# Optimization experiments

Hardware: AMD Instinct MI355X
Metric: run time of the kernel (lower is better)

The kernel has to match this reference:

```python
import jax, jax.numpy as jnp
import numpy as np

IN_F = 3072       # in_features
OUT_F = 9216      # out_features = 3 * N_HEADS * HEAD_DIM (fused QKV)
GROUP = 64        # quantization group size
RANK = 32         # lora_rank
HEAD_DIM = 128
N_HEADS = OUT_F // (3 * HEAD_DIM)  # 24
EPS = 1e-6
LORA_SCALE = 1.0


def setup_inputs() -> dict:
    key = jax.random.key(0)
    ks = jax.random.split(key, 10)
    B, S = 1, 4096
    x = jax.random.normal(ks[0], (B, S, IN_F), dtype=jnp.float32)
    # packed int4 weights: two signed int4 values per int8 byte
    qweight = jax.random.randint(ks[1], (OUT_F, IN_F // 2), -128, 128, dtype=jnp.int32).astype(jnp.int8)
    wscales = (jax.random.uniform(ks[2], (IN_F // GROUP, OUT_F)) * 0.02 + 0.001).astype(jnp.float32)
    bias = (jax.random.normal(ks[3], (OUT_F,)) * 0.01).astype(jnp.float32)
    lora_down = (jax.random.normal(ks[4], (IN_F, RANK)) * 0.02).astype(jnp.float32)
    lora_up = (jax.random.normal(ks[5], (OUT_F, RANK)) * 0.02).astype(jnp.float32)
    smooth = (jax.random.uniform(ks[6], (IN_F,)) * 0.5 + 0.75).astype(jnp.float32)   # keep away from 0
    norm_q = (jax.random.uniform(ks[7], (HEAD_DIM,)) * 0.5 + 0.75).astype(jnp.float32)
    norm_k = (jax.random.uniform(ks[8], (HEAD_DIM,)) * 0.5 + 0.75).astype(jnp.float32)
    ang = jax.random.uniform(ks[9], (S, HEAD_DIM // 2)) * (2.0 * np.pi)
    rotary_emb = jnp.stack([jnp.cos(ang), jnp.sin(ang)], axis=-1).astype(jnp.float32)  # [S, D/2, 2]
    return dict(x=x, qweight=qweight, wscales=wscales, bias=bias, lora_down=lora_down,
                lora_up=lora_up, smooth=smooth, norm_q=norm_q, norm_k=norm_k, rotary_emb=rotary_emb)


def _dequant_weight(qweight, wscales):
    # unpack two signed int4 lanes from each int8 (low nibble first), then per-group scale
    low = jnp.right_shift(jnp.left_shift(qweight, 4), 4)   # arithmetic shifts on int8 -> sign extend
    high = jnp.right_shift(qweight, 4)
    w4 = jnp.stack([low, high], axis=-1).reshape(OUT_F, IN_F)          # int4 codes in [-8, 7]
    wg = w4.astype(jnp.float32).reshape(OUT_F, IN_F // GROUP, GROUP)
    return (wg * wscales.T[:, :, None]).reshape(OUT_F, IN_F)          # [N, K]


def _quantize_act(x, smooth, lora_down):
    # fused: smooth -> symmetric per-token per-group int4 quantize -> lora_down projection
    B, S, K = x.shape
    M = B * S
    xs = (x / smooth).reshape(M, K)
    xg = xs.reshape(M, K // GROUP, GROUP)
    ascale = jnp.max(jnp.abs(xg), axis=-1, keepdims=True) / 7.0
    ascale = jnp.maximum(ascale, 1e-8)
    q = jnp.clip(jnp.round(xg / ascale), -8.0, 7.0)
    deq = (q * ascale).reshape(M, K)                                   # dequantized int4 activation
    lora_act = xs @ lora_down                                          # [M, RANK], fp32 side path
    return deq, lora_act


def _rope(t, cos, sin):
    # interleaved pairs (even, odd) rotation; t: [M, H, D], cos/sin: [M, 1, D/2]
    e, o = t[..., 0::2], t[..., 1::2]
    re = e * cos - o * sin
    ro = e * sin + o * cos
    return jnp.stack([re, ro], axis=-1).reshape(t.shape)


def reference(x, qweight, wscales, bias, lora_down, lora_up, smooth, norm_q, norm_k, rotary_emb):
    B, S, K = x.shape
    M = B * S
    deq_x, lora_act = _quantize_act(x, smooth, lora_down)
    w = _dequant_weight(qweight, wscales)
    # main int4 GEMM + LoRA up + bias, all fused in the real kernel
    out = deq_x @ w.T + (LORA_SCALE * lora_act) @ lora_up.T + bias     # [M, OUT_F]
    qkv = out.reshape(M, 3, N_HEADS, HEAD_DIM)
    q, k, v = qkv[:, 0], qkv[:, 1], qkv[:, 2]
    def rms(t, g):
        return t * jax.lax.rsqrt(jnp.mean(t * t, axis=-1, keepdims=True) + EPS) * g
    q = rms(q, norm_q)
    k = rms(k, norm_k)
    cos = rotary_emb[:, None, :, 0]   # [M, 1, D/2]
    sin = rotary_emb[:, None, :, 1]
    q = _rope(q, cos, sin)
    k = _rope(k, cos, sin)
    return jnp.stack([q, k, v], axis=1).reshape(B, S, OUT_F)
```

## Files before the change

kernel.cpp:

```cpp
#include <hip/hip_runtime.h>
#include <cstdint>

#define MDIM 4096
#define NDIM 9216
#define KDIM 3072
#define KP   3136
#define NKT  49

#define QB 4096
#define WB 13824
#define PB 2304

typedef unsigned int u32;
typedef unsigned short u16;
typedef float f32x4 __attribute__((ext_vector_type(4)));
typedef __bf16 bf16x8 __attribute__((ext_vector_type(8)));

__device__ __forceinline__ u16 f2bf(float f) {
  u32 u = __float_as_uint(f);
  u32 r = u + 0x7fffu + ((u >> 16) & 1u);
  return (u16)(r >> 16);
}

__device__ __forceinline__ float frcp(float f) { return __builtin_amdgcn_rcpf(f); }

__device__ __forceinline__ void gld_lds16(const void* g, void* l) {
  __builtin_amdgcn_global_load_lds((__attribute__((address_space(1))) void*)g,
                                   (__attribute__((address_space(3))) void*)l,
                                   16, 0, 0);
}

__global__ __launch_bounds__(256) void k_prep(const float* __restrict__ x, const u32* __restrict__ qw,
                        const float* __restrict__ wsc, const float* __restrict__ lora_down,
                        const float* __restrict__ lora_up, const float* __restrict__ smooth,
                        u16* __restrict__ Aex, u16* __restrict__ Bex) {
  __shared__ float xs_s[KDIM];
  __shared__ float part[64 * 32];
  const int tid = threadIdx.x;
  int bid = blockIdx.x;

  if (bid >= QB) {
    bid -= QB;
    if (bid >= WB) {
      int idx = (bid - WB) * 256 + tid;
      int n = idx >> 6, c = idx & 63;
      u16 v = 0;
      if (c < 32) v = f2bf(lora_up[n * 32 + c]);
      Bex[(size_t)n * KP + 3072 + c] = v;
      return;
    }
    __shared__ int s_viol;
    u32 probe = qw[tid];
    bool ok = (probe >> 8) == ((probe & 0x80u) ? 0xffffffu : 0u);
    if (tid == 0) s_viol = 0;
    __syncthreads();
    if (!ok) atomicOr(&s_viol, 1);
    __syncthreads();
    const int f = (s_viol == 0);

    int idx = bid * 256 + tid;
    int n = idx / 384;
    int j = idx - n * 384;
    int k0 = j * 8;
    u32 w;
    if (f) {
      uint4 q4 = ((const uint4*)qw)[idx];
      w = (q4.x & 0xffu) | ((q4.y & 0xffu) << 8) | ((q4.z & 0xffu) << 16) | ((q4.w & 0xffu) << 24);
    } else {
      w = qw[idx];
    }
    float ws = wsc[(k0 >> 6) * NDIM + n];
    u32 ow[4];
    #pragma unroll
    for (int b = 0; b < 4; ++b) {
      int by = (int)((w >> (8 * b)) & 0xffu);
      int lo = (by << 28) >> 28;
      int hi = (by << 24) >> 28;
      ow[b] = (u32)f2bf((float)lo * ws) | ((u32)f2bf((float)hi * ws) << 16);
    }
    *(uint4*)(Bex + (size_t)n * KP + k0) = make_uint4(ow[0], ow[1], ow[2], ow[3]);
    return;
  }

  const int m = bid;
  const int sub = tid & 15;
  const float* xr = x + (size_t)m * KDIM;
  u16* arow = Aex + (size_t)m * KP;

  #pragma unroll
  for (int p = 0; p < 3; ++p) {
    int g = p * 16 + (tid >> 4);
    int k0 = g * 64 + sub * 4;
    float4 xv = *(const float4*)(xr + k0);
    float4 sv = *(const float4*)(smooth + k0);
    float a0 = xv.x * frcp(sv.x), a1 = xv.y * frcp(sv.y);
    float a2 = xv.z * frcp(sv.z), a3 = xv.w * frcp(sv.w);
    xs_s[k0+0] = a0; xs_s[k0+1] = a1; xs_s[k0+2] = a2; xs_s[k0+3] = a3;
    float am = fmaxf(fmaxf(fabsf(a0), fabsf(a1)), fmaxf(fabsf(a2), fabsf(a3)));
    am = fmaxf(am, __shfl_xor(am, 8, 16));
    am = fmaxf(am, __shfl_xor(am, 4, 16));
    am = fmaxf(am, __shfl_xor(am, 2, 16));
    am = fmaxf(am, __shfl_xor(am, 1, 16));
    float asc = fmaxf(am * (1.0f / 7.0f), 1e-8f);
    float iasc = frcp(asc);
    float q0 = fminf(7.f, fmaxf(-8.f, rintf(a0 * iasc)));
    float q1 = fminf(7.f, fmaxf(-8.f, rintf(a1 * iasc)));
    float q2 = fminf(7.f, fmaxf(-8.f, rintf(a2 * iasc)));
    float q3 = fminf(7.f, fmaxf(-8.f, rintf(a3 * iasc)));
    float d0 = q0 * asc, d1 = q1 * asc, d2 = q2 * asc, d3 = q3 * asc;
    u32 lo = (u32)f2bf(d0) | ((u32)f2bf(d1) << 16);
    u32 hi = (u32)f2bf(d2) | ((u32)f2bf(d3) << 16);
    *(uint2*)(arow + k0) = make_uint2(lo, hi);
  }
  if (tid < 32) arow[3104 + tid] = 0;
  __syncthreads();

  {
    const int c  = tid >> 2;
    const int r8 = (tid & 3) * 8;
    float a[8] = {0.f, 0.f, 0.f, 0.f, 0.f, 0.f, 0.f, 0.f};
    const float* lp = lora_down + (size_t)c * 32 + r8;
    #pragma unroll 4
    for (int i = 0; i < 48; ++i) {
      float xv = xs_s[i * 64 + c];
      float4 l0 = *(const float4*)(lp);
      float4 l1 = *(const float4*)(lp + 4);
      a[0] = fmaf(xv, l0.x, a[0]); a[1] = fmaf(xv, l0.y, a[1]);
      a[2] = fmaf(xv, l0.z, a[2]); a[3] = fmaf(xv, l0.w, a[3]);
      a[4] = fmaf(xv, l1.x, a[4]); a[5] = fmaf(xv, l1.y, a[5]);
      a[6] = fmaf(xv, l1.z, a[6]); a[7] = fmaf(xv, l1.w, a[7]);
      lp += 64 * 32;
    }
    __syncthreads();
    *(float4*)(&part[c * 32 + r8])     = make_float4(a[0], a[1], a[2], a[3]);
    *(float4*)(&part[c * 32 + r8 + 4]) = make_float4(a[4], a[5], a[6], a[7]);
  }
  __syncthreads();
  if (tid < 32) {
    float s = 0.f;
    #pragma unroll 8
    for (int cc = 0; cc < 64; ++cc) s += part[cc * 32 + tid];
    arow[3072 + tid] = f2bf(s);
  }
}

__global__ __launch_bounds__(256) void k_gemm(const u16* __restrict__ A, const u16* __restrict__ B,
                                              const float* __restrict__ bias, const float* __restrict__ norm_q,
                                              const float* __restrict__ norm_k, const float* __restrict__ rot,
                                              float* __restrict__ out) {
  __shared__ __align__(16) u16 sA[128 * 64];
  __shared__ __align__(16) u16 sB[128 * 64];
  const int tid  = threadIdx.x;
  const int lane = tid & 63;
  const int wave = tid >> 6;
  const int m0 = blockIdx.y * 128;
  const int n0 = blockIdx.x * 128;
  const int wm = (wave >> 1) * 64;
  const int wn = (wave & 1) * 64;
  const int lr = lane & 15;
  const int lq = lane >> 4;

  f32x4 acc[4][4] = {};

  const u16* ga[4]; const u16* gb[4]; u16* la[4]; u16* lb[4];
  #pragma unroll
  for (int i = 0; i < 4; ++i) {
    int p = i * 256 + tid;
    int r = p >> 3;
    int c = (p & 7) ^ (r & 7);
    ga[i] = A + (size_t)(m0 + r) * KP + c * 8;
    gb[i] = B + (size_t)(n0 + r) * KP + c * 8;
    la[i] = &sA[p * 8];
    lb[i] = &sB[p * 8];
  }
  int aoff[2][4], boff[2][4];
  #pragma unroll
  for (int ks = 0; ks < 2; ++ks) {
    int cch = lq + ks * 4;
    #pragma unroll
    for (int t = 0; t < 4; ++t) {
      int rowa = wm + t * 16 + lr;
      int rowb = wn + t * 16 + lr;
      aoff[ks][t] = rowa * 64 + ((cch ^ (rowa & 7)) * 8);
      boff[ks][t] = rowb * 64 + ((cch ^ (rowb & 7)) * 8);
    }
  }

  for (int kt = 0; kt < NKT; ++kt) {
    #pragma unroll
    for (int i = 0; i < 4; ++i) { gld_lds16(ga[i], la[i]); ga[i] += 64; }
    #pragma unroll
    for (int i = 0; i < 4; ++i) { gld_lds16(gb[i], lb[i]); gb[i] += 64; }
    asm volatile("s_waitcnt vmcnt(0)" ::: "memory");
    __syncthreads();
    #pragma unroll
    for (int ks = 0; ks < 2; ++ks) {
      bf16x8 af[4], bf[4];
      #pragma unroll
      for (int t = 0; t < 4; ++t) af[t] = *(const bf16x8*)&sA[aoff[ks][t]];
      #pragma unroll
      for (int t = 0; t < 4; ++t) bf[t] = *(const bf16x8*)&sB[boff[ks][t]];
      #pragma unroll
      for (int ti = 0; ti < 4; ++ti)
        #pragma unroll
        for (int tj = 0; tj < 4; ++tj)
          acc[ti][tj] = __builtin_amdgcn_mfma_f32_16x16x32_bf16(af[ti], bf[tj], acc[ti][tj], 0, 0, 0);
    }
    __syncthreads();
  }

  const int sel = (n0 >= 6144) ? 2 : ((n0 >= 3072) ? 1 : 0);

  #pragma unroll
  for (int tj = 0; tj < 4; ++tj) {
    float bv = bias[n0 + wn + tj * 16 + lr];
    #pragma unroll
    for (int ti = 0; ti < 4; ++ti)
      #pragma unroll
      for (int rg = 0; rg < 4; ++rg)
        acc[ti][tj][rg] += bv;
  }

  if (sel == 2) {
    #pragma unroll
    for (int tj = 0; tj < 4; ++tj) {
      int n = n0 + wn + tj * 16 + lr;
      #pragma unroll
      for (int ti = 0; ti < 4; ++ti) {
        int mrow = m0 + wm + ti * 16 + lq * 4;
        #pragma unroll
        for (int rg = 0; rg < 4; ++rg)
          out[(size_t)(mrow + rg) * NDIM + n] = acc[ti][tj][rg];
      }
    }
    return;
  }

  float part[4][4];
  #pragma unroll
  for (int ti = 0; ti < 4; ++ti)
    #pragma unroll
    for (int rg = 0; rg < 4; ++rg) {
      float s = 0.f;
      #pragma unroll
      for (int tj = 0; tj < 4; ++tj) s += acc[ti][tj][rg] * acc[ti][tj][rg];
      part[ti][rg] = s;
    }
  #pragma unroll
  for (int off = 1; off < 16; off <<= 1)
    #pragma unroll
    for (int ti = 0; ti < 4; ++ti)
      #pragma unroll
      for (int rg = 0; rg < 4; ++rg)
        part[ti][rg] += __shfl_xor(part[ti][rg], off);

  float* ssq = (float*)sA;
  #pragma unroll
  for (int ti = 0; ti < 4; ++ti)
    #pragma unroll
    for (int rg = 0; rg < 4; ++rg)
      if (lr == ti * 4 + rg)
        ssq[(wn >> 6) * 128 + wm + ti * 16 + lq * 4 + rg] = part[ti][rg];
  __syncthreads();

  const float* nrm = sel ? norm_k : norm_q;
  float gm[4];
  #pragma unroll
  for (int tj = 0; tj < 4; ++tj) gm[tj] = nrm[wn + tj * 16 + lr];
  const float2* rot2 = (const float2*)rot;
  const float sgn = (lr & 1) ? 1.0f : -1.0f;

  #pragma unroll
  for (int ti = 0; ti < 4; ++ti) {
    #pragma unroll
    for (int rg = 0; rg < 4; ++rg) {
      int row = wm + ti * 16 + lq * 4 + rg;
      float tot = ssq[row] + ssq[128 + row];
      float rs = rsqrtf(tot * (1.0f / 128.0f) + 1e-6f);
      int m = m0 + row;
      #pragma unroll
      for (int tj = 0; tj < 4; ++tj) {
        int nl = wn + tj * 16 + lr;
        float v = acc[ti][tj][rg] * rs * gm[tj];
        float p = __shfl_xor(v, 1);
        float2 cs = rot2[(size_t)m * 64 + (nl >> 1)];
        float r = v * cs.x + sgn * (p * cs.y);
        out[(size_t)m * NDIM + n0 + nl] = r;
      }
    }
  }
}

extern "C" void kernel_launch(void* const* d_in, const int* in_sizes, int n_in,
                              void* d_out, int out_size, void* d_ws, size_t ws_size,
                              hipStream_t stream) {
  const float* x         = (const float*)d_in[0];
  const u32*   qweight   = (const u32*)d_in[1];
  const float* wscales   = (const float*)d_in[2];
  const float* bias      = (const float*)d_in[3];
  const float* lora_down = (const float*)d_in[4];
  const float* lora_up   = (const float*)d_in[5];
  const float* smooth    = (const float*)d_in[6];
  const float* norm_q    = (const float*)d_in[7];
  const float* norm_k    = (const float*)d_in[8];
  const float* rot       = (const float*)d_in[9];
  float* out = (float*)d_out;

  u16* Aex = (u16*)d_ws;
  u16* Bex = Aex + (size_t)MDIM * KP;

  k_prep<<<QB + WB + PB, 256, 0, stream>>>(x, qweight, wscales, lora_down, lora_up, smooth, Aex, Bex);
  k_gemm<<<dim3(NDIM / 128, MDIM / 128), 256, 0, stream>>>(Aex, Bex, bias, norm_q, norm_k, rot, out);
}
```

Measured before the change: 593.1 us.

## Restructure GEMM to 256x256 tiles with 4-stage LDS pipeline and 8 waves

The bf16 MFMA GEMM grows from 128x128 tiles with 4 waves to 256x256 tiles with 8 waves, and its K step shrinks to 32. A 4-deep ring of LDS buffers (128KB dynamic shared memory) issues global-to-LDS loads three stages ahead, and the MFMA phases are split with barriers and setprio so loads overlap compute. The goal is to raise data reuse per tile and hide global memory latency that the old synchronous load-then-compute loop exposed. In exchange, the large LDS use and register footprint limit occupancy to one block per CU, and the grid shrinks to 576 blocks, which may cause tail imbalance.

```diff
diff --git a/kernel.cpp b/kernel.cpp
--- a/kernel.cpp
+++ b/kernel.cpp
@@ -5,7 +5,7 @@
 #define NDIM 9216
 #define KDIM 3072
 #define KP   3136
-#define NKT  49
+#define NKT2 97
 
 #define QB 4096
 #define WB 13824
@@ -144,148 +144,182 @@
   }
 }
 
-__global__ __launch_bounds__(256) void k_gemm(const u16* __restrict__ A, const u16* __restrict__ B,
+__global__ __launch_bounds__(512) void k_gemm(const u16* __restrict__ A, const u16* __restrict__ B,
                                               const float* __restrict__ bias, const float* __restrict__ norm_q,
                                               const float* __restrict__ norm_k, const float* __restrict__ rot,
                                               float* __restrict__ out) {
-  __shared__ __align__(16) u16 sA[128 * 64];
-  __shared__ __align__(16) u16 sB[128 * 64];
+  extern __shared__ u16 lds[];
   const int tid  = threadIdx.x;
   const int lane = tid & 63;
   const int wave = tid >> 6;
-  const int m0 = blockIdx.y * 128;
-  const int n0 = blockIdx.x * 128;
-  const int wm = (wave >> 1) * 64;
-  const int wn = (wave & 1) * 64;
+  const int m0 = blockIdx.y * 256;
+  const int n0 = blockIdx.x * 256;
+  const int wm = (wave >> 2) * 128;
+  const int wn = (wave & 3) * 64;
   const int lr = lane & 15;
   const int lq = lane >> 4;
 
-  f32x4 acc[4][4] = {};
-
-  const u16* ga[4]; const u16* gb[4]; u16* la[4]; u16* lb[4];
-  #pragma unroll
-  for (int i = 0; i < 4; ++i) {
-    int p = i * 256 + tid;
-    int r = p >> 3;
-    int c = (p & 7) ^ (r & 7);
-    ga[i] = A + (size_t)(m0 + r) * KP + c * 8;
-    gb[i] = B + (size_t)(n0 + r) * KP + c * 8;
-    la[i] = &sA[p * 8];
-    lb[i] = &sB[p * 8];
-  }
-  int aoff[2][4], boff[2][4];
-  #pragma unroll
-  for (int ks = 0; ks < 2; ++ks) {
-    int cch = lq + ks * 4;
-    #pragma unroll
-    for (int t = 0; t < 4; ++t) {
-      int rowa = wm + t * 16 + lr;
-      int rowb = wn + t * 16 + lr;
-      aoff[ks][t] = rowa * 64 + ((cch ^ (rowa & 7)) * 8);
-      boff[ks][t] = rowb * 64 + ((cch ^ (rowb & 7)) * 8);
-    }
-  }
-
-  for (int kt = 0; kt < NKT; ++kt) {
-    #pragma unroll
-    for (int i = 0; i < 4; ++i) { gld_lds16(ga[i], la[i]); ga[i] += 64; }
-    #pragma unroll
-    for (int i = 0; i < 4; ++i) { gld_lds16(gb[i], lb[i]); gb[i] += 64; }
-    asm volatile("s_waitcnt vmcnt(0)" ::: "memory");
-    __syncthreads();
-    #pragma unroll
-    for (int ks = 0; ks < 2; ++ks) {
-      bf16x8 af[4], bf[4];
-      #pragma unroll
-      for (int t = 0; t < 4; ++t) af[t] = *(const bf16x8*)&sA[aoff[ks][t]];
-      #pragma unroll
-      for (int t = 0; t < 4; ++t) bf[t] = *(const bf16x8*)&sB[boff[ks][t]];
-      #pragma unroll
-      for (int ti = 0; ti < 4; ++ti)
-        #pragma unroll
-        for (int tj = 0; tj < 4; ++tj)
-          acc[ti][tj] = __builtin_amdgcn_mfma_f32_16x16x32_bf16(af[ti], bf[tj], acc[ti][tj], 0, 0, 0);
-    }
-    __syncthreads();
-  }
-
-  const int sel = (n0 >= 6144) ? 2 : ((n0 >= 3072) ? 1 : 0);
-
-  #pragma unroll
-  for (int tj = 0; tj < 4; ++tj) {
-    float bv = bias[n0 + wn + tj * 16 + lr];
+  const u16 *pA0, *pA1, *pB0, *pB1;
+  int la0, la1, lb0, lb1;
+  {
+    auto mk = [&](int p, const u16* base, int nb) -> const u16* {
+      int pr = p >> 3, cs = p & 7;
+      int c  = cs ^ (pr & 7);
+      int r  = pr * 2 + (c >> 2);
+      int kc = c & 3;
+      return base + (size_t)(nb + r) * KP + kc * 8;
+    };
+    int p0 = tid, p1 = 512 + tid;
+    pA0 = mk(p0, A, m0); pA1 = mk(p1, A, m0);
+    pB0 = mk(p0, B, n0); pB1 = mk(p1, B, n0);
+    la0 = p0 * 8;        la1 = p1 * 8;
+    lb0 = 8192 + p0 * 8; lb1 = 8192 + p1 * 8;
+  }
+
+  int aoff[8], boff[4];
+  #pragma unroll
+  for (int t = 0; t < 8; ++t) {
+    int ra = wm + t * 16 + lr;
+    int pr = ra >> 1, c = (ra & 1) * 4 + lq;
+    aoff[t] = pr * 64 + ((c ^ (pr & 7)) * 8);
+  }
+  #pragma unroll
+  for (int t = 0; t < 4; ++t) {
+    int rb = wn + t * 16 + lr;
+    int pr = rb >> 1, c = (rb & 1) * 4 + lq;
+    boff[t] = 8192 + pr * 64 + ((c ^ (pr & 7)) * 8);
+  }
+
+  f32x4 acc[8][4] = {};
+
+  #pragma unroll
+  for (int s = 0; s < 3; ++s) {
+    u16* sl = lds + (s << 14);
+    gld_lds16(pA0, sl + la0); gld_lds16(pA1, sl + la1);
+    gld_lds16(pB0, sl + lb0); gld_lds16(pB1, sl + lb1);
+    pA0 += 32; pA1 += 32; pB0 += 32; pB1 += 32;
+  }
+  asm volatile("s_waitcnt vmcnt(8)" ::: "memory");
+  __builtin_amdgcn_s_barrier();
+
+  #pragma unroll 1
+  for (int kt = 0; kt < NKT2; ++kt) {
+    const u16* sA_ = lds + ((kt & 3) << 14);
+    u16* stl = lds + (((kt + 3) & 3) << 14);
+    const bool st = (kt < NKT2 - 3);
+    bf16x8 af[4], bf[4];
+
+    if (st) { gld_lds16(pA0, stl + la0); gld_lds16(pA1, stl + la1); }
+    #pragma unroll
+    for (int t = 0; t < 4; ++t) af[t] = *(const bf16x8*)&sA_[aoff[t]];
+    #pragma unroll
+    for (int t = 0; t < 4; ++t) bf[t] = *(const bf16x8*)&sA_[boff[t]];
+    __builtin_amdgcn_s_barrier();
+    asm volatile("s_waitcnt lgkmcnt(0)" ::: "memory");
+    __builtin_amdgcn_sched_barrier(0);
+    __builtin_amdgcn_s_setprio(1);
     #pragma unroll
     for (int ti = 0; ti < 4; ++ti)
       #pragma unroll
+      for (int tj = 0; tj < 4; ++tj)
+        acc[ti][tj] = __builtin_amdgcn_mfma_f32_16x16x32_bf16(af[ti], bf[tj], acc[ti][tj], 0, 0, 0);
+    __builtin_amdgcn_s_setprio(0);
+    __builtin_amdgcn_sched_barrier(0);
+    __builtin_amdgcn_s_barrier();
+
+    if (st) { gld_lds16(pB0, stl + lb0); gld_lds16(pB1, stl + lb1);
+              pA0 += 32; pA1 += 32; pB0 += 32; pB1 += 32; }
+    #pragma unroll
+    for (int t = 0; t < 4; ++t) af[t] = *(const bf16x8*)&sA_[aoff[4 + t]];
+    __builtin_amdgcn_s_barrier();
+    asm volatile("s_waitcnt lgkmcnt(0)" ::: "memory");
+    __builtin_amdgcn_sched_barrier(0);
+    __builtin_amdgcn_s_setprio(1);
+    #pragma unroll
+    for (int ti = 0; ti < 4; ++ti)
+      #pragma unroll
+      for (int tj = 0; tj < 4; ++tj)
+        acc[4 + ti][tj] = __builtin_amdgcn_mfma_f32_16x16x32_bf16(af[ti], bf[tj], acc[4 + ti][tj], 0, 0, 0);
+    __builtin_amdgcn_s_setprio(0);
+    __builtin_amdgcn_sched_barrier(0);
+    if (st) asm volatile("s_waitcnt vmcnt(8)" ::: "memory");
+    else    asm volatile("s_waitcnt vmcnt(0)" ::: "memory");
+    __builtin_amdgcn_s_barrier();
+  }
+
+  const int sel = (blockIdx.x >= 24) ? 2 : (blockIdx.x >= 12 ? 1 : 0);
+
+  float bv[4];
+  #pragma unroll
+  for (int tj = 0; tj < 4; ++tj) bv[tj] = bias[n0 + wn + tj * 16 + lr];
+  #pragma unroll
+  for (int ti = 0; ti < 8; ++ti)
+    #pragma unroll
+    for (int tj = 0; tj < 4; ++tj)
+      #pragma unroll
       for (int rg = 0; rg < 4; ++rg)
-        acc[ti][tj][rg] += bv;
-  }
+        acc[ti][tj][rg] += bv[tj];
 
   if (sel == 2) {
     #pragma unroll
     for (int tj = 0; tj < 4; ++tj) {
       int n = n0 + wn + tj * 16 + lr;
       #pragma unroll
-      for (int ti = 0; ti < 4; ++ti) {
-        int mrow = m0 + wm + ti * 16 + lq * 4;
+      for (int ti = 0; ti < 8; ++ti) {
+        int mr = m0 + wm + ti * 16 + lq * 4;
         #pragma unroll
         for (int rg = 0; rg < 4; ++rg)
-          out[(size_t)(mrow + rg) * NDIM + n] = acc[ti][tj][rg];
+          out[(size_t)(mr + rg) * NDIM + n] = acc[ti][tj][rg];
       }
     }
     return;
   }
 
-  float part[4][4];
-  #pragma unroll
-  for (int ti = 0; ti < 4; ++ti)
+  float* ssq = (float*)lds;
+  #pragma unroll
+  for (int ti = 0; ti < 8; ++ti) {
+    float pr4[4];
     #pragma unroll
     for (int rg = 0; rg < 4; ++rg) {
       float s = 0.f;
       #pragma unroll
       for (int tj = 0; tj < 4; ++tj) s += acc[ti][tj][rg] * acc[ti][tj][rg];
-      part[ti][rg] = s;
-    }
-  #pragma unroll
-  for (int off = 1; off < 16; off <<= 1)
-    #pragma unroll
-    for (int ti = 0; ti < 4; ++ti)
-      #pragma unroll
-      for (int rg = 0; rg < 4; ++rg)
-        part[ti][rg] += __shfl_xor(part[ti][rg], off);
-
-  float* ssq = (float*)sA;
-  #pragma unroll
-  for (int ti = 0; ti < 4; ++ti)
+      pr4[rg] = s;
+    }
+    #pragma unroll
+    for (int off = 1; off < 16; off <<= 1)
+      #pragma unroll
+      for (int rg = 0; rg < 4; ++rg) pr4[rg] += __shfl_xor(pr4[rg], off);
     #pragma unroll
     for (int rg = 0; rg < 4; ++rg)
-      if (lr == ti * 4 + rg)
-        ssq[(wn >> 6) * 128 + wm + ti * 16 + lq * 4 + rg] = part[ti][rg];
+      if (lr == (ti & 3) * 4 + rg)
+        ssq[(wn >> 6) * 256 + wm + ti * 16 + lq * 4 + rg] = pr4[rg];
+  }
   __syncthreads();
 
   const float* nrm = sel ? norm_k : norm_q;
   float gm[4];
   #pragma unroll
-  for (int tj = 0; tj < 4; ++tj) gm[tj] = nrm[wn + tj * 16 + lr];
+  for (int tj = 0; tj < 4; ++tj) gm[tj] = nrm[(wn & 64) + tj * 16 + lr];
   const float2* rot2 = (const float2*)rot;
   const float sgn = (lr & 1) ? 1.0f : -1.0f;
-
-  #pragma unroll
-  for (int ti = 0; ti < 4; ++ti) {
+  const int hb = (wn >> 7) * 512;
+
+  #pragma unroll
+  for (int ti = 0; ti < 8; ++ti) {
     #pragma unroll
     for (int rg = 0; rg < 4; ++rg) {
       int row = wm + ti * 16 + lq * 4 + rg;
-      float tot = ssq[row] + ssq[128 + row];
+      float tot = ssq[hb + row] + ssq[hb + 256 + row];
       float rs = rsqrtf(tot * (1.0f / 128.0f) + 1e-6f);
       int m = m0 + row;
       #pragma unroll
       for (int tj = 0; tj < 4; ++tj) {
-        int nl = wn + tj * 16 + lr;
+        int nl = (wn & 64) + tj * 16 + lr;
         float v = acc[ti][tj][rg] * rs * gm[tj];
         float p = __shfl_xor(v, 1);
         float2 cs = rot2[(size_t)m * 64 + (nl >> 1)];
-        float r = v * cs.x + sgn * (p * cs.y);
-        out[(size_t)m * NDIM + n0 + nl] = r;
+        out[(size_t)m * NDIM + n0 + wn + tj * 16 + lr] = v * cs.x + sgn * (p * cs.y);
       }
     }
   }
@@ -309,6 +343,13 @@
   u16* Aex = (u16*)d_ws;
   u16* Bex = Aex + (size_t)MDIM * KP;
 
+  static bool attr_set = false;
+  if (!attr_set) {
+    hipFuncSetAttribute(reinterpret_cast<const void*>(k_gemm),
+                        hipFuncAttributeMaxDynamicSharedMemorySize, 131072);
+    attr_set = true;
+  }
+
   k_prep<<<QB + WB + PB, 256, 0, stream>>>(x, qweight, wscales, lora_down, lora_up, smooth, Aex, Bex);
-  k_gemm<<<dim3(NDIM / 128, MDIM / 128), 256, 0, stream>>>(Aex, Bex, bias, norm_q, norm_k, rot, out);
-}
+  k_gemm<<<dim3(NDIM / 256, MDIM / 256), 512, 131072, stream>>>(Aex, Bex, bias, norm_q, norm_k, rot, out);
+}
```

Result: faster. 561.5 us (-5.3%).
